# Optimization experiments

Hardware: AMD Instinct MI355X
Metric: run time of the kernel (lower is better)

## Reference

```python
import jax, jax.numpy as jnp
import numpy as np
import math

N = 64
DIN = 2
DOUT = 2
D = 4
BATCH = 16384
EPS_DIV = 1e-6


def setup_inputs() -> dict:
    key = jax.random.key(0)
    k1, k2, k3 = jax.random.split(key, 3)
    x = jax.random.normal(k1, (BATCH, N, DIN), jnp.float32)
    # A scaled by 0.5 to keep 64-step products of DxD matrices inside float32 range
    A = jax.random.normal(k2, (N, D, D, DIN), jnp.float32) * 0.5
    B = jax.random.normal(k3, (N, D, D, DOUT, DIN), jnp.float32)
    scale = jnp.ones((1,), jnp.float32)
    return {"x": x, "A": A, "B": B, "scale": scale}


def _forward(x, A, B, scale):
    b, n, din = x.shape
    nbin = int(math.log(n - 1) / math.log(2.0)) + 1  # matches torch set_parallel_vars
    s = scale.reshape(())
    # per-site L2 normalization of input features (torch: X / ||X||, no eps)
    xn = x / jnp.linalg.norm(x, axis=-1, keepdims=True)
    M = jnp.einsum('bni,nlri->nblr', xn, A)  # [n, b, D, D] site matrices
    # binary tree of pairwise products: levels[l] has (n >> l) blocks covering 2^l sites
    levels = [M]
    cur = M
    for _ in range(nbin - 1):
        m = cur.shape[0]
        pair = cur.reshape(m // 2, 2, b, D, D)
        cur = jnp.einsum('pbij,pbjk->pbik', pair[:, 0], pair[:, 1])
        levels.append(cur)
    idx = jnp.arange(n)
    # Left prefix boundary vectors: vL[i] = e0^T * prod_{k<i} M_k (i=0 unused).
    # Built by walking the set bits of i (MSB->LSB), exactly like the torch
    # Bleft[nbin-1-j][xp[j]] indexing, but vectorized over all i at once.
    vL = jnp.zeros((n, b, D), M.dtype)
    startedL = jnp.zeros((n,), bool)
    for j in range(nbin):
        l = nbin - 1 - j                 # tree level for bit j
        bit = ((idx >> l) & 1).astype(bool)
        blk = 2 * (idx >> (l + 1))       # == xp[j] in torch
        Bl = levels[l][blk]              # [n, b, D, D]
        init = Bl[:, :, 0, :]            # left boundary row e0^T A
        step = jnp.einsum('nbi,nbij->nbj', vL, Bl)
        new = jnp.where(startedL[:, None, None], step, init)
        vL = jnp.where(bit[:, None, None], new, vL)
        startedL = startedL | bit
    vL = vL / (jnp.linalg.norm(vL, axis=-1, keepdims=True) + EPS_DIV)
    # Right suffix boundary vectors: vR[i] = (prod_{k=n-i}^{n-1} M_k) e0 (i=0 unused).
    # For n a power of two, Bright levels coincide with Bleft levels.
    vR = jnp.zeros((n, b, D), M.dtype)
    startedR = jnp.zeros((n,), bool)
    for j in range(nbin):
        l = nbin - 1 - j
        bit = ((idx >> l) & 1).astype(bool)
        nblk = n >> l
        blk = nblk - 1 - 2 * (idx >> (l + 1))  # index from the right end
        Bl = levels[l][blk]
        init = Bl[:, :, :, 0]            # right boundary column A e0
        step = jnp.einsum('nbij,nbj->nbi', Bl, vR)
        new = jnp.where(startedR[:, None, None], step, init)
        vR = jnp.where(bit[:, None, None], new, vR)
        startedR = startedR | bit
    vR = vR / (jnp.linalg.norm(vR, axis=-1, keepdims=True) + EPS_DIV)
    Aright = vR[::-1]  # Aright[i] = vR[n-1-i], valid for sites 0..n-2
    # Local operators H_i: boundary-contracted MPO tensors
    Hmid = jnp.einsum('nbi,niljk,nbl->nbjk', vL[1:n - 1], B[1:n - 1], Aright[1:n - 1])
    H0 = jnp.einsum('ljk,bl->bjk', B[0, 0], Aright[0])
    Hlast = jnp.einsum('bi,ijk->bjk', vL[n - 1], B[n - 1, :, 0])
    H = jnp.concatenate([H0[None], Hmid, Hlast[None]], axis=0)  # [n, b, dout, din]
    nrm = jnp.sqrt(jnp.sum(H * H, axis=(-2, -1), keepdims=True)) + EPS_DIV
    H = s * (H / nrm)
    H = jnp.where(jnp.isnan(H), 0.0, H)
    H = jax.nn.relu(H)                   # activation='relu'
    # apply local operator to normalized local input; out_norm='none'
    y = jnp.einsum('nbjk,bnk->bnj', H, xn)  # [b, n, dout]
    return y


def reference(x, A, B, scale):
    return _forward(x, A, B, scale)
```

## Files before the change

kernel.cpp:

```cpp
#include <hip/hip_runtime.h>
#include <math.h>


#define EPS 1e-6f
#define RSQ(x) __builtin_amdgcn_rsqf((x) + 1e-30f)

__global__ __launch_bounds__(256)
void tdvp_kernel(const float* __restrict__ x,
                 const float* __restrict__ A,
                 const float* __restrict__ Bw,
                 const float* __restrict__ scale,
                 float* __restrict__ y)
{
    __shared__ float  sP[8 * 16 * 32];
    __shared__ float  sXY[32 * 130];
    __shared__ float4 sA[64 * 8];
    __shared__ float4 sB[64 * 16];

    const int tid = threadIdx.x;
    const int bb  = tid & 31;
    const int s   = tid >> 5;

    {
        const float4* xg = (const float4*)x + (size_t)blockIdx.x * 1024;
        #pragma unroll
        for (int it = 0; it < 4; ++it) {
            const int g = it * 256 + tid;
            const float4 v = xg[g];
            const int c = g >> 5, f = (g & 31) * 4;
            *(float2*)&sXY[c * 130 + f]     = make_float2(v.x, v.y);
            *(float2*)&sXY[c * 130 + f + 2] = make_float2(v.z, v.w);
        }
        const float4* Ag = (const float4*)A;
        #pragma unroll
        for (int it = 0; it < 2; ++it)
            sA[it * 256 + tid] = Ag[it * 256 + tid];
        const float4* Bg = (const float4*)Bw;
        #pragma unroll
        for (int it = 0; it < 4; ++it)
            sB[it * 256 + tid] = Bg[it * 256 + tid];
    }
    __syncthreads();

    const int n0 = s * 8;
    float xa[8], xc[8];
    #pragma unroll
    for (int k = 0; k < 8; ++k) {
        const float2 v = *(const float2*)&sXY[bb * 130 + s * 16 + 2 * k];
        const float inr = RSQ(v.x * v.x + v.y * v.y);
        xa[k] = v.x * inr; xc[k] = v.y * inr;
    }

    float M[8][16];
    #pragma unroll
    for (int k = 0; k < 8; ++k) {
        const float4* Aq = &sA[(n0 + k) * 8];
        #pragma unroll
        for (int t = 0; t < 8; ++t) {
            const float4 q = Aq[t];
            M[k][2*t]     = fmaf(xc[k], q.y, xa[k] * q.x);
            M[k][2*t + 1] = fmaf(xc[k], q.w, xa[k] * q.z);
        }
    }

    {
        float P[16];
        #pragma unroll
        for (int e = 0; e < 16; ++e) P[e] = M[0][e];
        #pragma unroll
        for (int k = 1; k < 8; ++k) {
            float Pn[16];
            #pragma unroll
            for (int i = 0; i < 4; ++i) {
                #pragma unroll
                for (int j = 0; j < 4; ++j) {
                    float acc = P[i*4] * M[k][j];
                    acc = fmaf(P[i*4+1], M[k][4+j],  acc);
                    acc = fmaf(P[i*4+2], M[k][8+j],  acc);
                    acc = fmaf(P[i*4+3], M[k][12+j], acc);
                    Pn[i*4+j] = acc;
                }
            }
            #pragma unroll
            for (int e = 0; e < 16; ++e) P[e] = Pn[e];
        }
        float ss = 0.f;
        #pragma unroll
        for (int e = 0; e < 16; ++e) ss = fmaf(P[e], P[e], ss);
        const float rn = RSQ(ss);
        #pragma unroll
        for (int e = 0; e < 16; ++e)
            sP[s * 512 + e * 32 + bb] = P[e] * rn;
    }
    __syncthreads();

    float v0 = 1.f, v1 = 0.f, v2 = 0.f, v3 = 0.f;
    #pragma unroll 1
    for (int t = 0; t < s; ++t) {
        const float* pp = &sP[t * 512 + bb];
        const float p0  = pp[0],      p1  = pp[32],     p2  = pp[64],     p3  = pp[96];
        const float p4  = pp[128],    p5  = pp[160],    p6  = pp[192],    p7  = pp[224];
        const float p8  = pp[256],    p9  = pp[288],    p10 = pp[320],    p11 = pp[352];
        const float p12 = pp[384],    p13 = pp[416],    p14 = pp[448],    p15 = pp[480];
        const float w0 = v0*p0 + v1*p4 + v2*p8  + v3*p12;
        const float w1 = v0*p1 + v1*p5 + v2*p9  + v3*p13;
        const float w2 = v0*p2 + v1*p6 + v2*p10 + v3*p14;
        const float w3 = v0*p3 + v1*p7 + v2*p11 + v3*p15;
        const float rn = RSQ(w0*w0 + w1*w1 + w2*w2 + w3*w3);
        v0 = w0*rn; v1 = w1*rn; v2 = w2*rn; v3 = w3*rn;
    }
    float u0 = 1.f, u1 = 0.f, u2 = 0.f, u3 = 0.f;
    #pragma unroll 1
    for (int t = 7; t > s; --t) {
        const float* pp = &sP[t * 512 + bb];
        const float p0  = pp[0],      p1  = pp[32],     p2  = pp[64],     p3  = pp[96];
        const float p4  = pp[128],    p5  = pp[160],    p6  = pp[192],    p7  = pp[224];
        const float p8  = pp[256],    p9  = pp[288],    p10 = pp[320],    p11 = pp[352];
        const float p12 = pp[384],    p13 = pp[416],    p14 = pp[448],    p15 = pp[480];
        const float w0 = p0*u0  + p1*u1  + p2*u2  + p3*u3;
        const float w1 = p4*u0  + p5*u1  + p6*u2  + p7*u3;
        const float w2 = p8*u0  + p9*u1  + p10*u2 + p11*u3;
        const float w3 = p12*u0 + p13*u1 + p14*u2 + p15*u3;
        const float rn = RSQ(w0*w0 + w1*w1 + w2*w2 + w3*w3);
        u0 = w0*rn; u1 = w1*rn; u2 = w2*rn; u3 = w3*rn;
    }

    float vlA[8], vlB[8], vlC[8], vlD[8];
    {
        float a0 = v0, a1 = v1, a2 = v2, a3 = v3;
        #pragma unroll
        for (int k = 0; k < 8; ++k) {
            vlA[k] = a0; vlB[k] = a1; vlC[k] = a2; vlD[k] = a3;
            if (k == 7) break;
            const float t0 = a0*M[k][0] + a1*M[k][4] + a2*M[k][8]  + a3*M[k][12];
            const float t1 = a0*M[k][1] + a1*M[k][5] + a2*M[k][9]  + a3*M[k][13];
            const float t2 = a0*M[k][2] + a1*M[k][6] + a2*M[k][10] + a3*M[k][14];
            const float t3 = a0*M[k][3] + a1*M[k][7] + a2*M[k][11] + a3*M[k][15];
            a0 = t0; a1 = t1; a2 = t2; a3 = t3;
        }
    }

    const float sc = scale[0];
    #pragma unroll
    for (int kk = 7; kk >= 0; --kk) {
        const int n = n0 + kk;

        const float arn = RSQ(u0*u0 + u1*u1 + u2*u2 + u3*u3);
        float aa0 = u0*arn, aa1 = u1*arn, aa2 = u2*arn, aa3 = u3*arn;
        if (n == 63) { aa0 = 1.f; aa1 = aa2 = aa3 = 0.f; }

        const float wn = RSQ(vlA[kk]*vlA[kk] + vlB[kk]*vlB[kk] +
                             vlC[kk]*vlC[kk] + vlD[kk]*vlD[kk]);
        float vv0 = vlA[kk]*wn, vv1 = vlB[kk]*wn, vv2 = vlC[kk]*wn, vv3 = vlD[kk]*wn;
        if (n == 0) { vv0 = 1.f; vv1 = vv2 = vv3 = 0.f; }

        const float vv[4] = {vv0, vv1, vv2, vv3};
        const float aa[4] = {aa0, aa1, aa2, aa3};
        const float4* Bq = &sB[n * 16];
        float H00 = 0.f, H01 = 0.f, H10 = 0.f, H11 = 0.f;
        #pragma unroll
        for (int half = 0; half < 2; ++half) {
            float4 bq[8];
            #pragma unroll
            for (int t = 0; t < 8; ++t) bq[t] = Bq[half * 8 + t];
            #pragma unroll
            for (int i2 = 0; i2 < 2; ++i2) {
                const int i = half * 2 + i2;
                #pragma unroll
                for (int l = 0; l < 4; ++l) {
                    const float  c = vv[i] * aa[l];
                    const float4 q = bq[i2 * 4 + l];
                    H00 = fmaf(c, q.x, H00);
                    H01 = fmaf(c, q.y, H01);
                    H10 = fmaf(c, q.z, H10);
                    H11 = fmaf(c, q.w, H11);
                }
            }
        }
        const float rh = sc * RSQ(H00*H00 + H01*H01 + H10*H10 + H11*H11);
        H00 *= rh; H01 *= rh; H10 *= rh; H11 *= rh;
        if (__builtin_isnan(H00)) H00 = 0.f;
        if (__builtin_isnan(H01)) H01 = 0.f;
        if (__builtin_isnan(H10)) H10 = 0.f;
        if (__builtin_isnan(H11)) H11 = 0.f;
        H00 = fmaxf(H00, 0.f); H01 = fmaxf(H01, 0.f);
        H10 = fmaxf(H10, 0.f); H11 = fmaxf(H11, 0.f);

        float2 yo;
        yo.x = fmaf(H01, xc[kk], H00 * xa[kk]);
        yo.y = fmaf(H11, xc[kk], H10 * xa[kk]);
        *(float2*)&sXY[bb * 130 + 2 * n] = yo;

        if (kk > 0) {
            const float t0 = M[kk][0]*u0  + M[kk][1]*u1  + M[kk][2]*u2  + M[kk][3]*u3;
            const float t1 = M[kk][4]*u0  + M[kk][5]*u1  + M[kk][6]*u2  + M[kk][7]*u3;
            const float t2 = M[kk][8]*u0  + M[kk][9]*u1  + M[kk][10]*u2 + M[kk][11]*u3;
            const float t3 = M[kk][12]*u0 + M[kk][13]*u1 + M[kk][14]*u2 + M[kk][15]*u3;
            u0 = t0; u1 = t1; u2 = t2; u3 = t3;
        }
    }
    __syncthreads();

    {
        float4* yg = (float4*)y + (size_t)blockIdx.x * 1024;
        #pragma unroll
        for (int it = 0; it < 4; ++it) {
            const int g = it * 256 + tid;
            const int c = g >> 5, f = (g & 31) * 4;
            const float2 a = *(const float2*)&sXY[c * 130 + f];
            const float2 b = *(const float2*)&sXY[c * 130 + f + 2];
            yg[g] = make_float4(a.x, a.y, b.x, b.y);
        }
    }
}

extern "C" void kernel_launch(void* const* d_in, const int* in_sizes, int n_in,
                              void* d_out, int out_size, void* d_ws, size_t ws_size,
                              hipStream_t stream) {
    const float* x     = (const float*)d_in[0];
    const float* A     = (const float*)d_in[1];
    const float* B     = (const float*)d_in[2];
    const float* scale = (const float*)d_in[3];
    float* yp = (float*)d_out;
    const int batch  = in_sizes[0] / 128;
    const int blocks = batch / 32;
    tdvp_kernel<<<blocks, 256, 0, stream>>>(x, A, B, scale, yp);
}
```

Before: 77.70 us.

## Use 64-sample wave-wide blocks, unify shared memory, read A/B via scalar loads

Each block now handles 64 batch samples with 512 threads, so every wavefront of 64 lanes covers one site segment across distinct samples, and the segment index is made wave-uniform with readfirstlane. A and B are no longer staged in LDS. They are read straight from global memory with uniform addresses, which should compile to scalar loads. One shared buffer is reused for the input, the prefix products and the output, with extra barriers between phases. This cuts the LDS footprint and the staging work, and launch bounds of 512,2 cap registers to allow two blocks per CU. The risk is register spilling from the large M array under the tighter register cap.

Result: no change. 77.75 us (+0.1%).

```diff
diff --git a/kernel.cpp b/kernel.cpp
--- a/kernel.cpp
+++ b/kernel.cpp
@@ -5,40 +5,29 @@
 #define EPS 1e-6f
 #define RSQ(x) __builtin_amdgcn_rsqf((x) + 1e-30f)
 
-__global__ __launch_bounds__(256)
+__global__ __launch_bounds__(512, 2)
 void tdvp_kernel(const float* __restrict__ x,
                  const float* __restrict__ A,
                  const float* __restrict__ Bw,
                  const float* __restrict__ scale,
                  float* __restrict__ y)
 {
-    __shared__ float  sP[8 * 16 * 32];
-    __shared__ float  sXY[32 * 130];
-    __shared__ float4 sA[64 * 8];
-    __shared__ float4 sB[64 * 16];
+    __shared__ float sU[8320];
 
     const int tid = threadIdx.x;
-    const int bb  = tid & 31;
-    const int s   = tid >> 5;
-
-    {
-        const float4* xg = (const float4*)x + (size_t)blockIdx.x * 1024;
+    const int bb  = tid & 63;
+    const int s   = __builtin_amdgcn_readfirstlane(tid >> 6);
+
+    {
+        const float4* xg = (const float4*)x + (size_t)blockIdx.x * 2048;
         #pragma unroll
         for (int it = 0; it < 4; ++it) {
-            const int g = it * 256 + tid;
+            const int g = it * 512 + tid;
             const float4 v = xg[g];
             const int c = g >> 5, f = (g & 31) * 4;
-            *(float2*)&sXY[c * 130 + f]     = make_float2(v.x, v.y);
-            *(float2*)&sXY[c * 130 + f + 2] = make_float2(v.z, v.w);
-        }
-        const float4* Ag = (const float4*)A;
-        #pragma unroll
-        for (int it = 0; it < 2; ++it)
-            sA[it * 256 + tid] = Ag[it * 256 + tid];
-        const float4* Bg = (const float4*)Bw;
-        #pragma unroll
-        for (int it = 0; it < 4; ++it)
-            sB[it * 256 + tid] = Bg[it * 256 + tid];
+            *(float2*)&sU[c * 130 + f]     = make_float2(v.x, v.y);
+            *(float2*)&sU[c * 130 + f + 2] = make_float2(v.z, v.w);
+        }
     }
     __syncthreads();
 
@@ -46,21 +35,19 @@
     float xa[8], xc[8];
     #pragma unroll
     for (int k = 0; k < 8; ++k) {
-        const float2 v = *(const float2*)&sXY[bb * 130 + s * 16 + 2 * k];
+        const float2 v = *(const float2*)&sU[bb * 130 + n0 * 2 + 2 * k];
         const float inr = RSQ(v.x * v.x + v.y * v.y);
         xa[k] = v.x * inr; xc[k] = v.y * inr;
     }
+    __syncthreads();
 
     float M[8][16];
     #pragma unroll
     for (int k = 0; k < 8; ++k) {
-        const float4* Aq = &sA[(n0 + k) * 8];
-        #pragma unroll
-        for (int t = 0; t < 8; ++t) {
-            const float4 q = Aq[t];
-            M[k][2*t]     = fmaf(xc[k], q.y, xa[k] * q.x);
-            M[k][2*t + 1] = fmaf(xc[k], q.w, xa[k] * q.z);
-        }
+        const float* Ak = A + (size_t)(n0 + k) * 32;
+        #pragma unroll
+        for (int e = 0; e < 16; ++e)
+            M[k][e] = fmaf(xc[k], Ak[2 * e + 1], xa[k] * Ak[2 * e]);
     }
 
     {
@@ -90,18 +77,18 @@
         const float rn = RSQ(ss);
         #pragma unroll
         for (int e = 0; e < 16; ++e)
-            sP[s * 512 + e * 32 + bb] = P[e] * rn;
+            sU[s * 1024 + e * 64 + bb] = P[e] * rn;
     }
     __syncthreads();
 
     float v0 = 1.f, v1 = 0.f, v2 = 0.f, v3 = 0.f;
     #pragma unroll 1
     for (int t = 0; t < s; ++t) {
-        const float* pp = &sP[t * 512 + bb];
-        const float p0  = pp[0],      p1  = pp[32],     p2  = pp[64],     p3  = pp[96];
-        const float p4  = pp[128],    p5  = pp[160],    p6  = pp[192],    p7  = pp[224];
-        const float p8  = pp[256],    p9  = pp[288],    p10 = pp[320],    p11 = pp[352];
-        const float p12 = pp[384],    p13 = pp[416],    p14 = pp[448],    p15 = pp[480];
+        const float* pp = &sU[t * 1024 + bb];
+        const float p0  = pp[0],      p1  = pp[64],     p2  = pp[128],    p3  = pp[192];
+        const float p4  = pp[256],    p5  = pp[320],    p6  = pp[384],    p7  = pp[448];
+        const float p8  = pp[512],    p9  = pp[576],    p10 = pp[640],    p11 = pp[704];
+        const float p12 = pp[768],    p13 = pp[832],    p14 = pp[896],    p15 = pp[960];
         const float w0 = v0*p0 + v1*p4 + v2*p8  + v3*p12;
         const float w1 = v0*p1 + v1*p5 + v2*p9  + v3*p13;
         const float w2 = v0*p2 + v1*p6 + v2*p10 + v3*p14;
@@ -112,11 +99,11 @@
     float u0 = 1.f, u1 = 0.f, u2 = 0.f, u3 = 0.f;
     #pragma unroll 1
     for (int t = 7; t > s; --t) {
-        const float* pp = &sP[t * 512 + bb];
-        const float p0  = pp[0],      p1  = pp[32],     p2  = pp[64],     p3  = pp[96];
-        const float p4  = pp[128],    p5  = pp[160],    p6  = pp[192],    p7  = pp[224];
-        const float p8  = pp[256],    p9  = pp[288],    p10 = pp[320],    p11 = pp[352];
-        const float p12 = pp[384],    p13 = pp[416],    p14 = pp[448],    p15 = pp[480];
+        const float* pp = &sU[t * 1024 + bb];
+        const float p0  = pp[0],      p1  = pp[64],     p2  = pp[128],    p3  = pp[192];
+        const float p4  = pp[256],    p5  = pp[320],    p6  = pp[384],    p7  = pp[448];
+        const float p8  = pp[512],    p9  = pp[576],    p10 = pp[640],    p11 = pp[704];
+        const float p12 = pp[768],    p13 = pp[832],    p14 = pp[896],    p15 = pp[960];
         const float w0 = p0*u0  + p1*u1  + p2*u2  + p3*u3;
         const float w1 = p4*u0  + p5*u1  + p6*u2  + p7*u3;
         const float w2 = p8*u0  + p9*u1  + p10*u2 + p11*u3;
@@ -139,6 +126,7 @@
             a0 = t0; a1 = t1; a2 = t2; a3 = t3;
         }
     }
+    __syncthreads();
 
     const float sc = scale[0];
     #pragma unroll
@@ -156,25 +144,18 @@
 
         const float vv[4] = {vv0, vv1, vv2, vv3};
         const float aa[4] = {aa0, aa1, aa2, aa3};
-        const float4* Bq = &sB[n * 16];
+        const float* Bn = Bw + (size_t)n * 64;
         float H00 = 0.f, H01 = 0.f, H10 = 0.f, H11 = 0.f;
         #pragma unroll
-        for (int half = 0; half < 2; ++half) {
-            float4 bq[8];
+        for (int i = 0; i < 4; ++i) {
             #pragma unroll
-            for (int t = 0; t < 8; ++t) bq[t] = Bq[half * 8 + t];
-            #pragma unroll
-            for (int i2 = 0; i2 < 2; ++i2) {
-                const int i = half * 2 + i2;
-                #pragma unroll
-                for (int l = 0; l < 4; ++l) {
-                    const float  c = vv[i] * aa[l];
-                    const float4 q = bq[i2 * 4 + l];
-                    H00 = fmaf(c, q.x, H00);
-                    H01 = fmaf(c, q.y, H01);
-                    H10 = fmaf(c, q.z, H10);
-                    H11 = fmaf(c, q.w, H11);
-                }
+            for (int l = 0; l < 4; ++l) {
+                const float c = vv[i] * aa[l];
+                const int   q = (i * 4 + l) * 4;
+                H00 = fmaf(c, Bn[q + 0], H00);
+                H01 = fmaf(c, Bn[q + 1], H01);
+                H10 = fmaf(c, Bn[q + 2], H10);
+                H11 = fmaf(c, Bn[q + 3], H11);
             }
         }
         const float rh = sc * RSQ(H00*H00 + H01*H01 + H10*H10 + H11*H11);
@@ -189,7 +170,7 @@
         float2 yo;
         yo.x = fmaf(H01, xc[kk], H00 * xa[kk]);
         yo.y = fmaf(H11, xc[kk], H10 * xa[kk]);
-        *(float2*)&sXY[bb * 130 + 2 * n] = yo;
+        *(float2*)&sU[bb * 130 + 2 * n] = yo;
 
         if (kk > 0) {
             const float t0 = M[kk][0]*u0  + M[kk][1]*u1  + M[kk][2]*u2  + M[kk][3]*u3;
@@ -202,13 +183,13 @@
     __syncthreads();
 
     {
-        float4* yg = (float4*)y + (size_t)blockIdx.x * 1024;
+        float4* yg = (float4*)y + (size_t)blockIdx.x * 2048;
         #pragma unroll
         for (int it = 0; it < 4; ++it) {
-            const int g = it * 256 + tid;
+            const int g = it * 512 + tid;
             const int c = g >> 5, f = (g & 31) * 4;
-            const float2 a = *(const float2*)&sXY[c * 130 + f];
-            const float2 b = *(const float2*)&sXY[c * 130 + f + 2];
+            const float2 a = *(const float2*)&sU[c * 130 + f];
+            const float2 b = *(const float2*)&sU[c * 130 + f + 2];
             yg[g] = make_float4(a.x, a.y, b.x, b.y);
         }
     }
@@ -223,6 +204,6 @@
     const float* scale = (const float*)d_in[3];
     float* yp = (float*)d_out;
     const int batch  = in_sizes[0] / 128;
-    const int blocks = batch / 32;
-    tdvp_kernel<<<blocks, 256, 0, stream>>>(x, A, B, scale, yp);
+    const int blocks = batch / 64;
+    tdvp_kernel<<<blocks, 512, 0, stream>>>(x, A, B, scale, yp);
 }
```
